# Kernel optimization log

Measured on AMD Instinct MI355X. Metric: run time of the kernel, lower is better.

Reference implementation:

```python
import jax, jax.numpy as jnp
import numpy as np

N = 100000      # nodes
E = 1600000     # edges (no self loops; GATv2Conv adds them)
D_NODE = 256    # node_embedding_depth
D_MSG = 128     # message_depth
D_RBF = 32      # radial_dim
H = 8           # heads
D_HEAD = D_MSG // H


def setup_inputs() -> dict:
    key = jax.random.key(0)
    ks = jax.random.split(key, 12)
    x = jax.random.normal(ks[0], (N, D_NODE), dtype=jnp.float32)
    rbf = jax.random.uniform(ks[1], (E, D_RBF), dtype=jnp.float32)
    # edges with no self loops: src = (dst + r) % N, r in [1, N)
    dst = jax.random.randint(ks[2], (E,), 0, N)
    r = jax.random.randint(ks[3], (E,), 1, N)
    src = (dst + r) % N
    edge_index = jnp.stack([src, dst]).astype(jnp.int64)
    batch = jnp.zeros((N,), dtype=jnp.int64)
    s = 0.05
    W_n2m = jax.random.normal(ks[4], (D_MSG, D_NODE), dtype=jnp.float32) * s
    W_r2m = jax.random.normal(ks[5], (D_MSG, D_RBF), dtype=jnp.float32) * s
    Wl = jax.random.normal(ks[6], (D_MSG, D_MSG), dtype=jnp.float32) * s
    bl = jnp.zeros((D_MSG,), dtype=jnp.float32)
    Wr = jax.random.normal(ks[7], (D_MSG, D_MSG), dtype=jnp.float32) * s
    br = jnp.zeros((D_MSG,), dtype=jnp.float32)
    We = jax.random.normal(ks[8], (D_MSG, D_MSG), dtype=jnp.float32) * s
    att = jax.random.normal(ks[9], (H, D_HEAD), dtype=jnp.float32) * s
    bias = jnp.zeros((D_MSG,), dtype=jnp.float32)
    W_m2n = jax.random.normal(ks[10], (D_NODE, D_MSG), dtype=jnp.float32) * s
    return {"x": x, "rbf": rbf, "edge_index": edge_index, "batch": batch,
            "W_n2m": W_n2m, "W_r2m": W_r2m, "Wl": Wl, "bl": bl, "Wr": Wr,
            "br": br, "We": We, "att": att, "bias": bias, "W_m2n": W_m2n}


def reference(x, rbf, edge_index, batch, W_n2m, W_r2m, Wl, bl, Wr, br, We, att, bias, W_m2n):
    n = x.shape[0]
    h, d = att.shape
    # node_to_message / radial_to_message (norm=None -> identity Normalization)
    xm = x @ W_n2m.T                      # [N, D_MSG]
    ea = rbf @ W_r2m.T                    # [E, D_MSG]
    src, dst = edge_index[0], edge_index[1]
    # GATv2Conv add_self_loops with fill_value='mean': self-loop edge_attr is
    # the mean of incoming edge attrs per target node (0 if none).
    deg = jax.ops.segment_sum(jnp.ones((ea.shape[0],), ea.dtype), dst, num_segments=n)
    loop_attr = jax.ops.segment_sum(ea, dst, num_segments=n) / jnp.maximum(deg, 1.0)[:, None]
    loop_idx = jnp.arange(n, dtype=src.dtype)
    src_f = jnp.concatenate([src, loop_idx])
    dst_f = jnp.concatenate([dst, loop_idx])
    ea_f = jnp.concatenate([ea, loop_attr], axis=0)   # [E+N, D_MSG]
    # GATv2 attention
    xl = (xm @ Wl.T + bl).reshape(n, h, d)            # source transform
    xr = (xm @ Wr.T + br).reshape(n, h, d)            # target transform
    e = (ea_f @ We.T).reshape(-1, h, d)               # edge transform
    u = jax.nn.leaky_relu(xl[src_f] + xr[dst_f] + e, 0.2)  # [E+N, H, d]
    logits = jnp.einsum('ehd,hd->eh', u, att)         # [E+N, H]
    # segment softmax over incoming edges per target node (self loops guarantee non-empty)
    mx = jax.ops.segment_max(logits, dst_f, num_segments=n)
    p = jnp.exp(logits - mx[dst_f])
    denom = jax.ops.segment_sum(p, dst_f, num_segments=n)
    alpha = p / denom[dst_f]                          # [E+N, H]
    msg = xl[src_f] * alpha[:, :, None]               # [E+N, H, d]
    out = jax.ops.segment_sum(msg, dst_f, num_segments=n).reshape(n, h * d) + bias
    return out @ W_m2n.T                              # [N, D_NODE]
```

## Files before the change

kernel.cpp:

```cpp
#include <hip/hip_runtime.h>
#include <cstdint>
#include <cstddef>

#define N_NODES 100000
#define N_EDGES 1600000

#define M_PAD 100096
#define SCAN_NB 98
#define CH 32

#define OFF_XLR    ((size_t)0)
#define OFF_XB     (OFF_XLR    + (size_t)N_NODES*256)
#define OFF_ACCB   (OFF_XB     + (size_t)12812288)
#define OFF_CSRS   (OFF_ACCB   + (size_t)6406144)
#define OFF_CSRE   (OFF_CSRS   + (size_t)N_EDGES)
#define OFF_ROW    (OFF_CSRE   + (size_t)N_EDGES)
#define OFF_CNT    (OFF_ROW    + (size_t)100016)
#define OFF_DEGI   (OFF_CNT    + (size_t)N_NODES)
#define OFF_BSUMS  (OFF_DEGI   + (size_t)N_NODES)
#define OFF_BCAT   (OFF_BSUMS  + 128)
#define OFF_WCOMBT (OFF_BCAT   + 256)
#define OFF_WCATB  (OFF_WCOMBT + 4096)
#define OFF_WM2NB  (OFF_WCATB  + 32768)

typedef __attribute__((ext_vector_type(8))) short short8;
typedef __attribute__((ext_vector_type(4))) float float4v;

__device__ __forceinline__ unsigned short f2bf(float f) {
  unsigned u = __float_as_uint(f);
  unsigned r = (u + 0x7fff + ((u >> 16) & 1)) >> 16;
  return (unsigned short)r;
}

__global__ void k_zero(float* __restrict__ p, size_t n4) {
  size_t i = (size_t)blockIdx.x * blockDim.x + threadIdx.x;
  size_t stride = (size_t)gridDim.x * blockDim.x;
  float4 z = make_float4(0.f, 0.f, 0.f, 0.f);
  for (; i < n4; i += stride) ((float4*)p)[i] = z;
}

__global__ void k_convx(const float* __restrict__ x, unsigned short* __restrict__ xb, unsigned n4) {
  unsigned i = blockIdx.x * blockDim.x + threadIdx.x;
  unsigned stride = gridDim.x * blockDim.x;
  for (; i < n4; i += stride) {
    float4 v = ((const float4*)x)[i];
    ushort4 o;
    o.x = f2bf(v.x); o.y = f2bf(v.y); o.z = f2bf(v.z); o.w = f2bf(v.w);
    ((ushort4*)xb)[i] = o;
  }
}

__global__ void k_weights(const float* __restrict__ Wl, const float* __restrict__ Wr,
                          const float* __restrict__ We, const float* __restrict__ W_n2m,
                          const float* __restrict__ W_r2m, const float* __restrict__ bl,
                          const float* __restrict__ br, const float* __restrict__ W_m2n,
                          unsigned short* __restrict__ WcatB, float* __restrict__ bcat,
                          float* __restrict__ WcombT, unsigned short* __restrict__ Wm2nB) {
  int idx = blockIdx.x * blockDim.x + threadIdx.x;
  if (idx < 65536) {
    int o = idx >> 8, i = idx & 255;
    const float* wrow = (o < 128) ? (Wl + o * 128) : (Wr + (o - 128) * 128);
    float s = 0.f;
    for (int k = 0; k < 128; ++k) s += wrow[k] * W_n2m[k * 256 + i];
    WcatB[idx] = f2bf(s);
  } else if (idx < 65536 + 256) {
    int o = idx - 65536;
    bcat[o] = (o < 128) ? bl[o] : br[o - 128];
  } else if (idx < 65536 + 256 + 4096) {
    int q = idx - (65536 + 256);
    int j = q >> 7, o = q & 127;
    float s = 0.f;
    for (int k = 0; k < 128; ++k) s += We[o * 128 + k] * W_r2m[k * 32 + j];
    WcombT[q] = s;
  } else if (idx < 65536 + 256 + 4096 + 32768) {
    int q = idx - (65536 + 256 + 4096);
    Wm2nB[q] = f2bf(W_m2n[q]);
  }
}

template <bool HAS_BIAS>
__global__ __launch_bounds__(256) void gemm_mfma(const unsigned short* __restrict__ A,
                                                 const unsigned short* __restrict__ B,
                                                 const float* __restrict__ bias,
                                                 float* __restrict__ C,
                                                 int M, int NC, int K) {
  __shared__ short As[128 * 32];
  __shared__ short Bs[128 * 32];
  const int tid = threadIdx.x;
  const int lane = tid & 63;
  const int wv = tid >> 6;
  const int rowBase = blockIdx.x << 7;
  const int colBase = blockIdx.y << 7;
  const int wrow = (wv & 1) << 6;
  const int wcol = (wv >> 1) << 6;

  const int srow = tid >> 2;
  const int skc = (tid & 3) << 3;

  const int n0 = lane & 15;
  const int q = lane >> 4;

  float4v acc[4][4];
#pragma unroll
  for (int i = 0; i < 4; ++i)
#pragma unroll
    for (int j = 0; j < 4; ++j) acc[i][j] = (float4v)(0.f);

  for (int k0 = 0; k0 < K; k0 += 32) {
    const unsigned aoff0 = (unsigned)(rowBase + srow) * K + k0 + skc;
    const unsigned aoff1 = (unsigned)(rowBase + 64 + srow) * K + k0 + skc;
    const unsigned boff0 = (unsigned)(colBase + srow) * K + k0 + skc;
    const unsigned boff1 = (unsigned)(colBase + 64 + srow) * K + k0 + skc;
    uint4 a0 = *(const uint4*)(A + aoff0);
    uint4 a1 = *(const uint4*)(A + aoff1);
    uint4 b0 = *(const uint4*)(B + boff0);
    uint4 b1 = *(const uint4*)(B + boff1);
    __syncthreads();
    ((uint4*)As)[tid] = a0;
    ((uint4*)As)[256 + tid] = a1;
    ((uint4*)Bs)[tid] = b0;
    ((uint4*)Bs)[256 + tid] = b1;
    __syncthreads();

    short8 af[4], bf[4];
    const short8* Ap = (const short8*)As;
    const short8* Bp = (const short8*)Bs;
#pragma unroll
    for (int i = 0; i < 4; ++i) af[i] = Ap[(wrow + i * 16 + n0) * 4 + q];
#pragma unroll
    for (int j = 0; j < 4; ++j) bf[j] = Bp[(wcol + j * 16 + n0) * 4 + q];
#pragma unroll
    for (int i = 0; i < 4; ++i)
#pragma unroll
      for (int j = 0; j < 4; ++j)
        acc[i][j] = __builtin_amdgcn_mfma_f32_16x16x32_bf16(af[i], bf[j], acc[i][j], 0, 0, 0);
  }

#pragma unroll
  for (int j = 0; j < 4; ++j) {
    const int col = colBase + wcol + j * 16 + n0;
    const float bv = HAS_BIAS ? bias[col] : 0.f;
#pragma unroll
    for (int i = 0; i < 4; ++i) {
      const int row0 = rowBase + wrow + i * 16 + (q << 2);
#pragma unroll
      for (int r = 0; r < 4; ++r) {
        const int row = row0 + r;
        if (row < M) C[(unsigned)row * NC + col] = acc[i][j][r] + bv;
      }
    }
  }
}

__global__ void k_hist(const int* __restrict__ dst, int* __restrict__ degi) {
  unsigned e = blockIdx.x * blockDim.x + threadIdx.x;
  if (e < N_EDGES) atomicAdd(&degi[dst[e]], 1);
}

__global__ __launch_bounds__(1024) void k_scan1(const int* __restrict__ degi,
                                                int* __restrict__ row,
                                                int* __restrict__ bsums) {
  __shared__ int sm[1024];
  const int tid = threadIdx.x;
  const unsigned i = blockIdx.x * 1024 + tid;
  int v = (i < N_NODES) ? degi[i] : 0;
  sm[tid] = v;
  __syncthreads();
  for (int d = 1; d < 1024; d <<= 1) {
    int t = (tid >= d) ? sm[tid - d] : 0;
    __syncthreads();
    sm[tid] += t;
    __syncthreads();
  }
  int incl = sm[tid];
  if (i < N_NODES) row[i] = incl - v;
  if (tid == 1023) bsums[blockIdx.x] = incl;
}

__global__ void k_scan2(int* __restrict__ bsums) {
  __shared__ int sm[SCAN_NB];
  const int tid = threadIdx.x;
  if (tid < SCAN_NB) sm[tid] = bsums[tid];
  __syncthreads();
  if (tid == 0) {
    int run = 0;
    for (int b = 0; b < SCAN_NB; ++b) { int t = sm[b]; sm[b] = run; run += t; }
  }
  __syncthreads();
  if (tid < SCAN_NB) bsums[tid] = sm[tid];
}

__global__ __launch_bounds__(1024) void k_scan3(int* __restrict__ row,
                                                const int* __restrict__ bsums) {
  const unsigned i = blockIdx.x * 1024 + threadIdx.x;
  if (i < N_NODES) row[i] += bsums[blockIdx.x];
  if (i == 0) row[N_NODES] = N_EDGES;
}

__global__ void k_scatter(const int* __restrict__ src, const int* __restrict__ dst,
                          const int* __restrict__ row, int* __restrict__ cnt,
                          int* __restrict__ csrs, int* __restrict__ csre) {
  unsigned e = blockIdx.x * blockDim.x + threadIdx.x;
  if (e < N_EDGES) {
    int d = dst[e];
    int pos = row[d] + atomicAdd(&cnt[d], 1);
    csrs[pos] = src[e];
    csre[pos] = (int)e;
  }
}

__global__ __launch_bounds__(128) void k_node(
    const float* __restrict__ XLR, const float* __restrict__ rbf,
    const int* __restrict__ csrs, const int* __restrict__ csre,
    const int* __restrict__ row, const float* __restrict__ WcombT,
    const float* __restrict__ att, const float* __restrict__ bias,
    unsigned short* __restrict__ accb) {
  __shared__ __align__(16) float rbf_s[CH][32];
  __shared__ int src_s[CH];
  __shared__ int eid_s[CH];
  __shared__ __align__(16) float rbfs_l[32];
  const int tid = threadIdx.x;
  const unsigned n = blockIdx.x;

  float wreg[32];
#pragma unroll
  for (int j = 0; j < 32; ++j) wreg[j] = WcombT[j * 128 + tid];
  const float att_r = att[tid];

  const int off = row[n], end = row[n + 1];
  const float xl_d = XLR[(n << 8) + tid];
  const float xr_d = XLR[(n << 8) + 128 + tid];

  float S = 0.f, den = 0.f;
  float rbfacc = 0.f;

  for (int c0 = off; c0 < end; c0 += CH) {
    const int cnt = min(CH, end - c0);
    __syncthreads();
    if (tid < cnt) { src_s[tid] = csrs[c0 + tid]; eid_s[tid] = csre[c0 + tid]; }
    __syncthreads();
    for (int idx = tid; idx < cnt * 32; idx += 128)
      rbf_s[idx >> 5][idx & 31] = rbf[(size_t)(unsigned)eid_s[idx >> 5] * 32 + (idx & 31)];
    __syncthreads();
#pragma unroll 2
    for (int i = 0; i < cnt; ++i) {
      const unsigned s = (unsigned)src_s[i];
      const float4* r4 = (const float4*)rbf_s[i];
      float et = 0.f;
#pragma unroll
      for (int j4 = 0; j4 < 8; ++j4) {
        float4 rv = r4[j4];
        et += rv.x * wreg[j4 * 4 + 0] + rv.y * wreg[j4 * 4 + 1] +
              rv.z * wreg[j4 * 4 + 2] + rv.w * wreg[j4 * 4 + 3];
      }
      const float xls = XLR[(s << 8) + tid];
      float u = xls + xr_d + et;
      u = (u > 0.f) ? u : 0.2f * u;
      float r = u * att_r;
      r += __shfl_xor(r, 1);
      r += __shfl_xor(r, 2);
      r += __shfl_xor(r, 4);
      r += __shfl_xor(r, 8);
      const float p = __expf(r);
      den += p;
      S += p * xls;
      if (tid < 32) rbfacc += rbf_s[i][tid];
    }
  }

  __syncthreads();
  if (tid < 32) rbfs_l[tid] = rbfacc;
  __syncthreads();
  const float inv = 1.f / fmaxf((float)(end - off), 1.f);
  float et = 0.f;
  {
    const float4* r4 = (const float4*)rbfs_l;
#pragma unroll
    for (int j4 = 0; j4 < 8; ++j4) {
      float4 rv = r4[j4];
      et += rv.x * wreg[j4 * 4 + 0] + rv.y * wreg[j4 * 4 + 1] +
            rv.z * wreg[j4 * 4 + 2] + rv.w * wreg[j4 * 4 + 3];
    }
  }
  et *= inv;
  float u = xl_d + xr_d + et;
  u = (u > 0.f) ? u : 0.2f * u;
  float r = u * att_r;
  r += __shfl_xor(r, 1);
  r += __shfl_xor(r, 2);
  r += __shfl_xor(r, 4);
  r += __shfl_xor(r, 8);
  const float p = __expf(r);
  den += p;
  S += p * xl_d;

  const float outv = S / den + bias[tid];
  accb[((size_t)n << 7) + tid] = f2bf(outv);
}

extern "C" void kernel_launch(void* const* d_in, const int* in_sizes, int n_in,
                              void* d_out, int out_size, void* d_ws, size_t ws_size,
                              hipStream_t stream) {
  const float* x     = (const float*)d_in[0];
  const float* rbf   = (const float*)d_in[1];
  const int*   ei    = (const int*)d_in[2];
  const float* W_n2m = (const float*)d_in[4];
  const float* W_r2m = (const float*)d_in[5];
  const float* Wl    = (const float*)d_in[6];
  const float* bl    = (const float*)d_in[7];
  const float* Wr    = (const float*)d_in[8];
  const float* br    = (const float*)d_in[9];
  const float* We    = (const float*)d_in[10];
  const float* att   = (const float*)d_in[11];
  const float* bias  = (const float*)d_in[12];
  const float* W_m2n = (const float*)d_in[13];
  float* out = (float*)d_out;
  float* ws  = (float*)d_ws;

  const int* src = ei;
  const int* dst = ei + N_EDGES;

  float* XLR    = ws + OFF_XLR;
  unsigned short* xb    = (unsigned short*)(ws + OFF_XB);
  unsigned short* accb  = (unsigned short*)(ws + OFF_ACCB);
  int* csrs   = (int*)(ws + OFF_CSRS);
  int* csre   = (int*)(ws + OFF_CSRE);
  int* rowoff = (int*)(ws + OFF_ROW);
  int* cnt    = (int*)(ws + OFF_CNT);
  int* degi   = (int*)(ws + OFF_DEGI);
  int* bsums  = (int*)(ws + OFF_BSUMS);
  float* bcat   = ws + OFF_BCAT;
  float* WcombT = ws + OFF_WCOMBT;
  unsigned short* WcatB = (unsigned short*)(ws + OFF_WCATB);
  unsigned short* Wm2nB = (unsigned short*)(ws + OFF_WM2NB);

  k_weights<<<401, 256, 0, stream>>>(Wl, Wr, We, W_n2m, W_r2m, bl, br, W_m2n,
                                     WcatB, bcat, WcombT, Wm2nB);
  k_convx<<<2048, 256, 0, stream>>>(x, xb, (unsigned)(N_NODES * 256 / 4));
  gemm_mfma<true><<<dim3(M_PAD / 128, 2), 256, 0, stream>>>(
      xb, WcatB, bcat, XLR, N_NODES, 256, 256);
  k_zero<<<196, 256, 0, stream>>>(ws + OFF_CNT, 50000);
  k_hist<<<N_EDGES / 256, 256, 0, stream>>>(dst, degi);
  k_scan1<<<SCAN_NB, 1024, 0, stream>>>(degi, rowoff, bsums);
  k_scan2<<<1, 128, 0, stream>>>(bsums);
  k_scan3<<<SCAN_NB, 1024, 0, stream>>>(rowoff, bsums);
  k_scatter<<<N_EDGES / 256, 256, 0, stream>>>(src, dst, rowoff, cnt, csrs, csre);
  k_node<<<N_NODES, 128, 0, stream>>>(XLR, rbf, csrs, csre, rowoff, WcombT,
                                      att, bias, accb);
  gemm_mfma<false><<<dim3(M_PAD / 128, 2), 256, 0, stream>>>(
      accb, Wm2nB, nullptr, out, N_NODES, 256, 128);
}
```

Measured before the change: 1.188 ms.

## Compute per-edge RBF projection with bf16 MFMA in node kernel

Replaces the per-thread 32-term scalar dot product for the edge attribute projection with a 16x16x32 bf16 MFMA over chunks of 16 edges. The result goes through shared memory, and the fused weight is now stored as bf16. The self-loop mean is computed by accumulating projected edge terms instead of raw RBF sums, and the 32 weight registers per thread are dropped. The aim is to cut VALU work and register pressure, at the cost of bf16 rounding on the rbf inputs and weights and a smaller chunk size.

```diff
diff --git a/kernel.cpp b/kernel.cpp
--- a/kernel.cpp
+++ b/kernel.cpp
@@ -7,7 +7,7 @@
 
 #define M_PAD 100096
 #define SCAN_NB 98
-#define CH 32
+#define CH 16
 
 #define OFF_XLR    ((size_t)0)
 #define OFF_XB     (OFF_XLR    + (size_t)N_NODES*256)
@@ -19,8 +19,8 @@
 #define OFF_DEGI   (OFF_CNT    + (size_t)N_NODES)
 #define OFF_BSUMS  (OFF_DEGI   + (size_t)N_NODES)
 #define OFF_BCAT   (OFF_BSUMS  + 128)
-#define OFF_WCOMBT (OFF_BCAT   + 256)
-#define OFF_WCATB  (OFF_WCOMBT + 4096)
+#define OFF_WCOMBB (OFF_BCAT   + 256)
+#define OFF_WCATB  (OFF_WCOMBB + 2048)
 #define OFF_WM2NB  (OFF_WCATB  + 32768)
 
 typedef __attribute__((ext_vector_type(8))) short short8;
@@ -55,7 +55,7 @@
                           const float* __restrict__ W_r2m, const float* __restrict__ bl,
                           const float* __restrict__ br, const float* __restrict__ W_m2n,
                           unsigned short* __restrict__ WcatB, float* __restrict__ bcat,
-                          float* __restrict__ WcombT, unsigned short* __restrict__ Wm2nB) {
+                          unsigned short* __restrict__ WcombB, unsigned short* __restrict__ Wm2nB) {
   int idx = blockIdx.x * blockDim.x + threadIdx.x;
   if (idx < 65536) {
     int o = idx >> 8, i = idx & 255;
@@ -71,7 +71,7 @@
     int j = q >> 7, o = q & 127;
     float s = 0.f;
     for (int k = 0; k < 128; ++k) s += We[o * 128 + k] * W_r2m[k * 32 + j];
-    WcombT[q] = s;
+    WcombB[o * 32 + j] = f2bf(s);
   } else if (idx < 65536 + 256 + 4096 + 32768) {
     int q = idx - (65536 + 256 + 4096);
     Wm2nB[q] = f2bf(W_m2n[q]);
@@ -212,47 +212,61 @@
 __global__ __launch_bounds__(128) void k_node(
     const float* __restrict__ XLR, const float* __restrict__ rbf,
     const int* __restrict__ csrs, const int* __restrict__ csre,
-    const int* __restrict__ row, const float* __restrict__ WcombT,
+    const int* __restrict__ row, const unsigned short* __restrict__ WcombB,
     const float* __restrict__ att, const float* __restrict__ bias,
     unsigned short* __restrict__ accb) {
-  __shared__ __align__(16) float rbf_s[CH][32];
+  __shared__ __align__(16) float et_s[CH][132];
   __shared__ int src_s[CH];
   __shared__ int eid_s[CH];
-  __shared__ __align__(16) float rbfs_l[32];
   const int tid = threadIdx.x;
+  const int lane = tid & 63;
+  const int wv = tid >> 6;
+  const int n0 = lane & 15;
+  const int q = lane >> 4;
+  const int wcol = wv << 6;
   const unsigned n = blockIdx.x;
 
-  float wreg[32];
-#pragma unroll
-  for (int j = 0; j < 32; ++j) wreg[j] = WcombT[j * 128 + tid];
   const float att_r = att[tid];
-
   const int off = row[n], end = row[n + 1];
   const float xl_d = XLR[(n << 8) + tid];
   const float xr_d = XLR[(n << 8) + 128 + tid];
 
-  float S = 0.f, den = 0.f;
-  float rbfacc = 0.f;
+  short8 bfr[4];
+#pragma unroll
+  for (int j = 0; j < 4; ++j)
+    bfr[j] = *(const short8*)(WcombB + (wcol + j * 16 + n0) * 32 + (q << 3));
+
+  float S = 0.f, den = 0.f, etacc = 0.f;
 
   for (int c0 = off; c0 < end; c0 += CH) {
     const int cnt = min(CH, end - c0);
     __syncthreads();
     if (tid < cnt) { src_s[tid] = csrs[c0 + tid]; eid_s[tid] = csre[c0 + tid]; }
     __syncthreads();
-    for (int idx = tid; idx < cnt * 32; idx += 128)
-      rbf_s[idx >> 5][idx & 31] = rbf[(size_t)(unsigned)eid_s[idx >> 5] * 32 + (idx & 31)];
+    short8 af = (short8)0;
+    if (n0 < cnt) {
+      const float* rp = rbf + (size_t)(unsigned)eid_s[n0] * 32 + (q << 3);
+      float4 v0 = ((const float4*)rp)[0];
+      float4 v1 = ((const float4*)rp)[1];
+      af[0] = (short)f2bf(v0.x); af[1] = (short)f2bf(v0.y);
+      af[2] = (short)f2bf(v0.z); af[3] = (short)f2bf(v0.w);
+      af[4] = (short)f2bf(v1.x); af[5] = (short)f2bf(v1.y);
+      af[6] = (short)f2bf(v1.z); af[7] = (short)f2bf(v1.w);
+    }
+    float4v c[4];
+#pragma unroll
+    for (int j = 0; j < 4; ++j)
+      c[j] = __builtin_amdgcn_mfma_f32_16x16x32_bf16(af, bfr[j], (float4v)(0.f), 0, 0, 0);
+#pragma unroll
+    for (int j = 0; j < 4; ++j)
+#pragma unroll
+      for (int r = 0; r < 4; ++r)
+        et_s[(q << 2) + r][wcol + j * 16 + n0] = c[j][r];
     __syncthreads();
 #pragma unroll 2
     for (int i = 0; i < cnt; ++i) {
       const unsigned s = (unsigned)src_s[i];
-      const float4* r4 = (const float4*)rbf_s[i];
-      float et = 0.f;
-#pragma unroll
-      for (int j4 = 0; j4 < 8; ++j4) {
-        float4 rv = r4[j4];
-        et += rv.x * wreg[j4 * 4 + 0] + rv.y * wreg[j4 * 4 + 1] +
-              rv.z * wreg[j4 * 4 + 2] + rv.w * wreg[j4 * 4 + 3];
-      }
+      const float et = et_s[i][tid];
       const float xls = XLR[(s << 8) + tid];
       float u = xls + xr_d + et;
       u = (u > 0.f) ? u : 0.2f * u;
@@ -264,26 +278,12 @@
       const float p = __expf(r);
       den += p;
       S += p * xls;
-      if (tid < 32) rbfacc += rbf_s[i][tid];
+      etacc += et;
     }
   }
 
-  __syncthreads();
-  if (tid < 32) rbfs_l[tid] = rbfacc;
-  __syncthreads();
   const float inv = 1.f / fmaxf((float)(end - off), 1.f);
-  float et = 0.f;
-  {
-    const float4* r4 = (const float4*)rbfs_l;
-#pragma unroll
-    for (int j4 = 0; j4 < 8; ++j4) {
-      float4 rv = r4[j4];
-      et += rv.x * wreg[j4 * 4 + 0] + rv.y * wreg[j4 * 4 + 1] +
-            rv.z * wreg[j4 * 4 + 2] + rv.w * wreg[j4 * 4 + 3];
-    }
-  }
-  et *= inv;
-  float u = xl_d + xr_d + et;
+  float u = xl_d + xr_d + etacc * inv;
   u = (u > 0.f) ? u : 0.2f * u;
   float r = u * att_r;
   r += __shfl_xor(r, 1);
@@ -330,12 +330,12 @@
   int* degi   = (int*)(ws + OFF_DEGI);
   int* bsums  = (int*)(ws + OFF_BSUMS);
   float* bcat   = ws + OFF_BCAT;
-  float* WcombT = ws + OFF_WCOMBT;
+  unsigned short* WcombB = (unsigned short*)(ws + OFF_WCOMBB);
   unsigned short* WcatB = (unsigned short*)(ws + OFF_WCATB);
   unsigned short* Wm2nB = (unsigned short*)(ws + OFF_WM2NB);
 
   k_weights<<<401, 256, 0, stream>>>(Wl, Wr, We, W_n2m, W_r2m, bl, br, W_m2n,
-                                     WcatB, bcat, WcombT, Wm2nB);
+                                     WcatB, bcat, WcombB, Wm2nB);
   k_convx<<<2048, 256, 0, stream>>>(x, xb, (unsigned)(N_NODES * 256 / 4));
   gemm_mfma<true><<<dim3(M_PAD / 128, 2), 256, 0, stream>>>(
       xb, WcatB, bcat, XLR, N_NODES, 256, 256);
@@ -345,7 +345,7 @@
   k_scan2<<<1, 128, 0, stream>>>(bsums);
   k_scan3<<<SCAN_NB, 1024, 0, stream>>>(rowoff, bsums);
   k_scatter<<<N_EDGES / 256, 256, 0, stream>>>(src, dst, rowoff, cnt, csrs, csre);
-  k_node<<<N_NODES, 128, 0, stream>>>(XLR, rbf, csrs, csre, rowoff, WcombT,
+  k_node<<<N_NODES, 128, 0, stream>>>(XLR, rbf, csrs, csre, rowoff, WcombB,
                                       att, bias, accb);
   gemm_mfma<false><<<dim3(M_PAD / 128, 2), 256, 0, stream>>>(
       accb, Wm2nB, nullptr, out, N_NODES, 256, 128);
```

Result: faster. 965.3 us (-18.7%).
